# Kernel tuning notes

Hardware: AMD Instinct MI355X
Metric: run time of the kernel (lower is better)

The kernel has to match this reference:

```python
import jax, jax.numpy as jnp
import numpy as np

# ---- Cl(3,0) geometric-algebra Cayley table (8 blades: 1,e1,e2,e3,e12,e13,e23,e123) ----
# T[k, i, j] = sign s.t. blade_i * blade_j = sign * blade_k (exactly 8 (i,j) pairs per k).

def _build_cayley():
    masks = [0b000, 0b001, 0b010, 0b100, 0b011, 0b101, 0b110, 0b111]
    T = np.zeros((8, 8, 8), np.float32)
    for i, a in enumerate(masks):
        for j, b in enumerate(masks):
            k = masks.index(a ^ b)
            aa, s = a >> 1, 0
            while aa:
                s += bin(aa & b).count('1')
                aa >>= 1
            T[k, i, j] = -1.0 if (s & 1) else 1.0
    return jnp.asarray(T)

CAYLEY = _build_cayley()
LN_EPS = 1e-5  # torch LayerNorm default


def _layer_norm(x, w, b):
    mu = jnp.mean(x, axis=-1, keepdims=True)
    var = jnp.var(x, axis=-1, keepdims=True)
    return (x - mu) * jax.lax.rsqrt(var + LN_EPS) * w + b


def _expert_forward(x_e, p_in, p_out, iw, gg, w_gate, w_up, w_down, lnw, lnb, out_w, out_b):
    # x_e: (C, D); p_in: (D, ED); per-round params indexed [r]
    C = x_e.shape[0]
    DB = lnw.shape[-1]
    mv = (x_e @ p_in).reshape(C, 8, DB)  # (C, n_blades, d_blade)
    n_rounds = iw.shape[0]
    for r in range(n_rounds):
        w = jax.nn.sigmoid(iw[r]).reshape(8, 8)          # interaction weights w[i,j]
        gate = jax.nn.sigmoid(gg[r])                      # scalar geo gate
        # geo[n,k,d] = sum_{i,j} sign[k,i,j] * w[i,j] * mv[n,i,d] * mv[n,j,d]
        geo = jnp.einsum('kij,ij,nid,njd->nkd', CAYLEY, w, mv, mv)
        mixed = gate * geo + (1.0 - gate) * mv
        flat = _layer_norm(mixed, lnw[r], lnb[r])         # LN over d_blade
        h = jax.nn.silu(flat @ w_gate[r]) * (flat @ w_up[r])  # SwiGLU
        mv = mv + h @ w_down[r]                           # residual
    out = mv.reshape(C, -1) @ p_out                       # (C, D)
    return _layer_norm(out, out_w, out_b)


def setup_inputs() -> dict:
    key = jax.random.key(0)
    ks = jax.random.split(key, 8)
    E, D, NB, DB, R, F = 16, 1024, 8, 64, 2, 256
    ED = NB * DB
    N = 32768
    C = N // E
    std = 0.02
    return {
        'x_sorted': jax.random.normal(ks[0], (N, D), jnp.float32),
        'proj_in': jax.random.normal(ks[1], (E, D, ED), jnp.float32) * std,
        'proj_out': jax.random.normal(ks[2], (E, ED, D), jnp.float32) * std,
        'interaction_weights': jnp.ones((E, R, 64), jnp.float32) * 0.1,
        'geo_gates': jnp.ones((E, R), jnp.float32) * 0.5,
        'ffn_gate': jax.random.normal(ks[3], (E, R, DB, F), jnp.float32) * std,
        'ffn_up': jax.random.normal(ks[4], (E, R, DB, F), jnp.float32) * std,
        'ffn_down': jax.random.normal(ks[5], (E, R, F, DB), jnp.float32) * std,
        'ffn_ln_w': jnp.ones((E, R, DB), jnp.float32),
        'ffn_ln_b': jnp.zeros((E, R, DB), jnp.float32),
        'out_ln_w': jnp.ones((D,), jnp.float32),
        'out_ln_b': jnp.zeros((D,), jnp.float32),
        'expert_offsets': jnp.arange(E, dtype=jnp.int32) * C,
        'expert_counts': jnp.full((E,), C, dtype=jnp.int32),
    }


def reference(x_sorted, proj_in, proj_out, interaction_weights, geo_gates,
              ffn_gate, ffn_up, ffn_down, ffn_ln_w, ffn_ln_b,
              out_ln_w, out_ln_b, expert_offsets, expert_counts):
    E = proj_in.shape[0]
    N, D = x_sorted.shape
    C = N // E  # balanced routing: equal tokens per expert (static shapes)
    idx = expert_offsets[:, None].astype(jnp.int32) + jnp.arange(C, dtype=jnp.int32)[None, :]
    x_b = x_sorted[idx]  # (E, C, D) gather of sorted tokens per expert
    y_b = jax.vmap(_expert_forward,
                   in_axes=(0, 0, 0, 0, 0, 0, 0, 0, 0, 0, None, None))(
        x_b, proj_in, proj_out, interaction_weights, geo_gates,
        ffn_gate, ffn_up, ffn_down, ffn_ln_w, ffn_ln_b, out_ln_w, out_ln_b)
    y = jnp.zeros_like(x_sorted).at[idx.reshape(-1)].set(y_b.reshape(-1, D))
    return y
```

## Files before the change

kernel.cpp:

```cpp
#include <hip/hip_runtime.h>

#define DEV __device__ __forceinline__

typedef __attribute__((ext_vector_type(4))) float f32x4;
typedef __attribute__((ext_vector_type(2))) float f32x2;
typedef __attribute__((ext_vector_type(8))) short bf16x8;


DEV unsigned short f2bf(float f) {
  union { float f; unsigned u; } v; v.f = f;
  unsigned r = v.u + 0x7fffu + ((v.u >> 16) & 1u);
  return (unsigned short)(r >> 16);
}

DEV unsigned pk2bf(float lo, float hi) {
  unsigned r;
  asm("v_cvt_pk_bf16_f32 %0, %1, %2" : "=v"(r) : "v"(lo), "v"(hi));
  return r;
}
DEV unsigned short f2bf1(float v) { return (unsigned short)pk2bf(v, v); }

DEV float bf2f(unsigned short b) {
  union { unsigned u; float f; } v; v.u = ((unsigned)b) << 16; return v.f;
}

DEV float frcp(float x) { return __builtin_amdgcn_rcpf(x); }

DEV void sbar() { asm volatile("s_barrier" ::: "memory"); }
DEV void wait_lgkm0() { asm volatile("s_waitcnt lgkmcnt(0)" ::: "memory"); }
DEV void wait_vm0() { asm volatile("s_waitcnt vmcnt(0)" ::: "memory"); }

DEV void async16(const unsigned short* g, unsigned short* l) {
  __builtin_amdgcn_global_load_lds(
      (__attribute__((address_space(1))) const unsigned int*)g,
      (__attribute__((address_space(3))) unsigned int*)l, 16, 0, 0);
}

DEV long tiled_off(long n, int k, int K) {
  return (n >> 3) * (8L * K) + (long)(((k >> 3) * 64) + ((int)(n & 7)) * 8 + (k & 7));
}

DEV bf16x8 ld_frag(const char* s, int row, int hi) {
  return *(const bf16x8*)(s + ((row >> 3) * 512 + hi * 128 + (row & 7) * 16));
}

__host__ __device__ constexpr int km_(int i) { return i==0?0:i==1?1:i==2?2:i==3?4:i==4?3:i==5?5:i==6?6:7; }
__host__ __device__ constexpr int pc_(int x) { int c = 0; while (x) { c += x & 1; x >>= 1; } return c; }
__host__ __device__ constexpr int KIDX(int i, int j) { return km_(km_(i) ^ km_(j)); }
__host__ __device__ constexpr int CSGN(int i, int j) {
  int a = km_(i), b = km_(j), aa = a >> 1, s = 0;
  while (aa) { s += pc_(aa & b); aa >>= 1; }
  return (s & 1) ? -1 : 1;
}
__host__ __device__ constexpr int PIDX(int i, int j) {
  return 8 * i - (i * (i - 1)) / 2 + (j - i);
}


DEV void geoprep_body(const float* __restrict__ iw, const float* __restrict__ gg,
                      float* __restrict__ wcomb, int er) {
  const float* w = iw + er * 64;
  float gate = frcp(1.f + __expf(-gg[er]));
  float* c = wcomb + er * 40;
  int p = 0;
  for (int i = 0; i < 8; ++i)
    for (int j = i; j < 8; ++j) {
      float v = (float)CSGN(i, j) * frcp(1.f + __expf(-w[i * 8 + j]));
      if (j > i) v += (float)CSGN(j, i) * frcp(1.f + __expf(-w[j * 8 + i]));
      c[p++] = gate * v;
    }
  c[36] = 1.f - gate;
}

template<int TI>
DEV void transpose_body(const float* __restrict__ in, unsigned short* __restrict__ out,
                        int Rr, int Cc, int bx, int by, int bz, int tid, char* sbuf) {
  unsigned short (*tile)[33] = (unsigned short (*)[33])sbuf;
  const float* ib = in + (long)bz * Rr * Cc;
  unsigned short* ob = out + (long)bz * Rr * Cc;
  int r0 = by * 32, c0 = bx * 32;
  int tr = tid >> 5, tc = tid & 31;
#pragma unroll
  for (int i = 0; i < 4; ++i) {
    int r = tr + i * 8;
    tile[r][tc] = f2bf(ib[(long)(r0 + r) * Cc + c0 + tc]);
  }
  __syncthreads();
#pragma unroll
  for (int i = 0; i < 4; ++i) {
    int c = tr + i * 8;
    int row = c0 + c;
    int k = r0 + tc;
    if (TI == 0) ob[(long)row * Rr + k] = tile[tc][c];
    else ob[(long)row * Rr + (k ^ ((row & 7) << 3))] = tile[tc][c];
  }
}

DEV void trans_big_body(const float* __restrict__ in, unsigned short* __restrict__ out,
                        int Rr, int Cc, int bx, int by, int bz, int tid, char* sbuf) {
  float (*t)[64] = (float (*)[64])sbuf;
  const float* ib = in + (long)bz * Rr * Cc;
  unsigned short* ob = out + (long)bz * (long)Rr * Cc;
  int k0 = by * 64, n0 = bx * 64;
#pragma unroll
  for (int p = 0; p < 4; ++p) {
    int idx = p * 256 + tid;
    int kr = idx >> 4, nc = (idx & 15) * 4;
    *(float4*)&t[kr][nc] = *(const float4*)(ib + (long)(k0 + kr) * Cc + n0 + nc);
  }
  __syncthreads();
#pragma unroll
  for (int p = 0; p < 2; ++p) {
    int idx = p * 256 + tid;
    int n = idx & 63, kc = idx >> 6;
    float v[8];
#pragma unroll
    for (int u = 0; u < 8; ++u) v[u] = t[kc * 8 + u][n];
    uint4 o;
    o.x = pk2bf(v[0], v[1]); o.y = pk2bf(v[2], v[3]);
    o.z = pk2bf(v[4], v[5]); o.w = pk2bf(v[6], v[7]);
    *(uint4*)(ob + tiled_off(n0 + n, k0 + kc * 8, Rr)) = o;
  }
}

__global__ __launch_bounds__(256) void prep_k(
    const float* __restrict__ pin, const float* __restrict__ pout,
    const float* __restrict__ fg, const float* __restrict__ fu,
    const float* __restrict__ fd, const float* __restrict__ iw,
    const float* __restrict__ gg,
    unsigned short* __restrict__ pinT, unsigned short* __restrict__ poutT,
    unsigned short* __restrict__ wgT, unsigned short* __restrict__ wuT,
    unsigned short* __restrict__ wdT, float* __restrict__ wcomb) {
  __shared__ char sbuf[16384];
  int b = blockIdx.x, tid = threadIdx.x;
  if (b < 2048) {
    trans_big_body(pin, pinT, 1024, 512, b & 7, (b >> 3) & 15, b >> 7, tid, sbuf);
  } else if (b < 4096) {
    int j = b - 2048;
    trans_big_body(pout, poutT, 512, 1024, j & 15, (j >> 4) & 7, j >> 7, tid, sbuf);
  } else if (b < 4608) {
    int j = b - 4096;
    transpose_body<1>(fg, wgT, 64, 256, j & 7, (j >> 3) & 1, j >> 4, tid, sbuf);
  } else if (b < 5120) {
    int j = b - 4608;
    transpose_body<1>(fu, wuT, 64, 256, j & 7, (j >> 3) & 1, j >> 4, tid, sbuf);
  } else if (b < 5632) {
    int j = b - 5120;
    transpose_body<0>(fd, wdT, 256, 64, j & 1, (j >> 1) & 7, j >> 4, tid, sbuf);
  } else {
    if (tid < 32) geoprep_body(iw, gg, wcomb, tid);
  }
}

__global__ __launch_bounds__(512, 1) void gemm_in_k(const float* __restrict__ X,
                                                    const unsigned short* __restrict__ Bw,
                                                    unsigned short* __restrict__ MvB,
                                                    const int* __restrict__ offs) {
  extern __shared__ char smem[];
  int bid = blockIdx.x;
  int wg = (bid & 7) * 32 + (bid >> 3);
  int e = wg >> 4, rem = wg & 15, bm = rem >> 1, bn = rem & 1;
  int tid = threadIdx.x, wid = tid >> 6, lane = tid & 63;
  int wm = (wid >> 2) * 128, wn = (wid & 3) * 64;
  int ri = lane & 15, hi = lane >> 4;
  long rowbase = (long)offs[e] + bm * 256;
  long bw = (long)e * 64 + bn * 32;

  auto STGB = [&](int p) {
    int t = p >> 1, s = p & 1, b = t & 1;
    char* dst = smem + b * 65536 + 32768 + s * 16384;
#pragma unroll
    for (int i = 0; i < 2; ++i) {
      int d = i * 512 + tid;
      async16(Bw + (bw + (d >> 5)) * 8192 +
                  (long)((t * 8 + s * 4 + ((d >> 3) & 3)) * 64 + (d & 7) * 8),
              (unsigned short*)(dst + d * 16));
    }
  };
  auto A_LOAD = [&](int p, float4 ar[2][2]) {
    int t = p >> 1, s = p & 1;
#pragma unroll
    for (int i = 0; i < 2; ++i) {
      int d = i * 512 + tid;
      const float* src = X + (rowbase + ((d >> 5) * 8 + (d & 7))) * 1024 +
                         t * 64 + s * 32 + ((d >> 3) & 3) * 8;
      ar[i][0] = *(const float4*)src;
      ar[i][1] = *(const float4*)(src + 4);
    }
  };
  auto A_WRITE = [&](int p, float4 ar[2][2]) {
    int t = p >> 1, s = p & 1, b = t & 1;
    char* dst = smem + b * 65536 + s * 16384;
#pragma unroll
    for (int i = 0; i < 2; ++i) {
      int d = i * 512 + tid;
      uint4 o;
      o.x = pk2bf(ar[i][0].x, ar[i][0].y);
      o.y = pk2bf(ar[i][0].z, ar[i][0].w);
      o.z = pk2bf(ar[i][1].x, ar[i][1].y);
      o.w = pk2bf(ar[i][1].z, ar[i][1].w);
      *(uint4*)(dst + d * 16) = o;
    }
  };

  f32x4 acc[8][4];
#pragma unroll
  for (int i = 0; i < 8; ++i)
#pragma unroll
    for (int j = 0; j < 4; ++j) acc[i][j] = (f32x4){0.f, 0.f, 0.f, 0.f};

  float4 ar[2][2];
  A_LOAD(0, ar); STGB(0); STGB(1);
  A_WRITE(0, ar);
  A_LOAD(1, ar);
  A_WRITE(1, ar);
  wait_lgkm0();

#pragma unroll 2
  for (int p = 0; p < 32; ++p) {
    int t = p >> 1, s = p & 1, c = t & 1;
    if (p < 30) { A_LOAD(p + 2, ar); STGB(p + 2); }
    if (p < 30) asm volatile("s_waitcnt vmcnt(8)" ::: "memory");
    else if (p == 30) asm volatile("s_waitcnt vmcnt(2)" ::: "memory");
    else asm volatile("s_waitcnt vmcnt(0)" ::: "memory");
    sbar();
    const char* cA = smem + c * 65536 + s * 16384;
    const char* cB = smem + c * 65536 + 32768 + s * 16384;
    bf16x8 a[8], b[4];
#pragma unroll
    for (int i = 0; i < 8; ++i) a[i] = ld_frag(cA, wm + i * 16 + ri, hi);
#pragma unroll
    for (int j = 0; j < 4; ++j) b[j] = ld_frag(cB, wn + j * 16 + ri, hi);
    __builtin_amdgcn_s_setprio(1);
#pragma unroll
    for (int i = 0; i < 8; ++i)
#pragma unroll
      for (int j = 0; j < 4; ++j)
        acc[i][j] = __builtin_amdgcn_mfma_f32_16x16x32_bf16(a[i], b[j], acc[i][j], 0, 0, 0);
    __builtin_amdgcn_s_setprio(0);
    if (p < 30) A_WRITE(p + 2, ar);
    wait_lgkm0();
  }

  unsigned short* Cb = MvB + ((long)e * 2048 + (long)bm * 256) * 512 + bn * 256;
#pragma unroll
  for (int i = 0; i < 8; ++i)
#pragma unroll
    for (int j = 0; j < 4; ++j)
#pragma unroll
      for (int rr = 0; rr < 4; ++rr)
        Cb[(long)(wm + i * 16 + hi * 4 + rr) * 512 + wn + j * 16 + ri] =
            f2bf1(acc[i][j][rr]);
}

__global__ __launch_bounds__(256, 2) void rounds_k(
    const unsigned short* __restrict__ MvB, const unsigned short* __restrict__ WgT,
    const unsigned short* __restrict__ WuT, const unsigned short* __restrict__ WdT,
    const float* __restrict__ wcomb, const float* __restrict__ lnw,
    const float* __restrict__ lnb, unsigned short* __restrict__ Mvb) {
  extern __shared__ char smem[];
  int tid = threadIdx.x, wid = tid >> 6, lane = tid & 63;
  char* sFH = smem + wid * 8192;
  char* sMv = smem + 32768 + wid * 8192;
  char* sW  = smem + 65536;

  int bid = blockIdx.x;
  int wg = (bid & 7) * 128 + (bid >> 3);
  int e = wg >> 6, bx = wg & 63;

  int t8 = lane >> 3, q = lane & 7;
  int ri = lane & 15, hi = lane >> 4;
  int sw = (ri & 7) << 4;

  auto STAGE = [&](int i8) {
    long base = (long)(e * 2 + (i8 >> 3)) * 16384 + (i8 & 7) * 2048;
    char* dst = sW + (i8 & 1) * 8192;
    async16(WgT + base + tid * 8, (unsigned short*)(dst + tid * 16));
    async16(WuT + base + tid * 8, (unsigned short*)(dst + 4096 + tid * 16));
  };
  STAGE(0);

#pragma unroll 1
  for (int r = 0; r < 2; ++r) {
    int er = e * 2 + r;
    const unsigned short* wd = WdT + (long)er * 16384;

    f32x4 mv[2][8];
    if (r == 0) {
      long base = ((long)e * 2048 + bx * 32 + wid * 8 + t8) * 512 + 8 * q;
      uint4 uv[8];
#pragma unroll
      for (int i = 0; i < 8; ++i)
        uv[i] = *(const uint4*)(MvB + base + i * 64);
#pragma unroll
      for (int i = 0; i < 8; ++i) {
        *(uint4*)(sMv + t8 * 1024 + i * 128 + ((16 * q) ^ (i << 4))) = uv[i];
        mv[0][i] = (f32x4){bf2f((unsigned short)(uv[i].x & 0xffff)),
                           bf2f((unsigned short)(uv[i].x >> 16)),
                           bf2f((unsigned short)(uv[i].y & 0xffff)),
                           bf2f((unsigned short)(uv[i].y >> 16))};
        mv[1][i] = (f32x4){bf2f((unsigned short)(uv[i].z & 0xffff)),
                           bf2f((unsigned short)(uv[i].z >> 16)),
                           bf2f((unsigned short)(uv[i].w & 0xffff)),
                           bf2f((unsigned short)(uv[i].w >> 16))};
      }
    } else {
#pragma unroll
      for (int i = 0; i < 8; ++i) {
        uint4 uv = *(const uint4*)(sMv + t8 * 1024 + i * 128 + ((16 * q) ^ (i << 4)));
        mv[0][i] = (f32x4){bf2f((unsigned short)(uv.x & 0xffff)),
                           bf2f((unsigned short)(uv.x >> 16)),
                           bf2f((unsigned short)(uv.y & 0xffff)),
                           bf2f((unsigned short)(uv.y >> 16))};
        mv[1][i] = (f32x4){bf2f((unsigned short)(uv.z & 0xffff)),
                           bf2f((unsigned short)(uv.z >> 16)),
                           bf2f((unsigned short)(uv.w & 0xffff)),
                           bf2f((unsigned short)(uv.w >> 16))};
      }
    }

    {
      const float* C = wcomb + er * 40;
      f32x4 g[2][8];
#pragma unroll
      for (int hf = 0; hf < 2; ++hf)
#pragma unroll
        for (int k = 0; k < 8; ++k) g[hf][k] = (f32x4){0.f, 0.f, 0.f, 0.f};
#pragma unroll
      for (int i = 0; i < 8; ++i)
#pragma unroll
        for (int j = i; j < 8; ++j) {
          float cc = C[PIDX(i, j)];
          const int k = KIDX(i, j);
          g[0][k] += cc * (mv[0][i] * mv[0][j]);
          g[1][k] += cc * (mv[1][i] * mv[1][j]);
        }
      float omg = C[36];
#pragma unroll
      for (int hf = 0; hf < 2; ++hf)
#pragma unroll
        for (int k = 0; k < 8; ++k) g[hf][k] = omg * mv[hf][k] + g[hf][k];
      float4 lwa = *(const float4*)(lnw + (long)er * 64 + 8 * q);
      float4 lwb = *(const float4*)(lnw + (long)er * 64 + 8 * q + 4);
      float4 lba = *(const float4*)(lnb + (long)er * 64 + 8 * q);
      float4 lbb = *(const float4*)(lnb + (long)er * 64 + 8 * q + 4);
      f32x4 lwvA = (f32x4){lwa.x, lwa.y, lwa.z, lwa.w};
      f32x4 lwvB = (f32x4){lwb.x, lwb.y, lwb.z, lwb.w};
      f32x4 lbvA = (f32x4){lba.x, lba.y, lba.z, lba.w};
      f32x4 lbvB = (f32x4){lbb.x, lbb.y, lbb.z, lbb.w};
#pragma unroll
      for (int bh = 0; bh < 2; ++bh) {
        f32x2 red[4];
#pragma unroll
        for (int k = 0; k < 4; ++k) {
          f32x4 a = g[0][bh * 4 + k], b = g[1][bh * 4 + k];
          red[k].x = ((a.x + a.y) + (a.z + a.w)) + ((b.x + b.y) + (b.z + b.w));
          red[k].y = (fmaf(a.x, a.x, a.y * a.y) + fmaf(a.z, a.z, a.w * a.w)) +
                     (fmaf(b.x, b.x, b.y * b.y) + fmaf(b.z, b.z, b.w * b.w));
        }
#pragma unroll
        for (int off = 4; off >= 1; off >>= 1)
#pragma unroll
          for (int t = 0; t < 4; ++t) {
            f32x2 o;
            o.x = __shfl_xor(red[t].x, off);
            o.y = __shfl_xor(red[t].y, off);
            red[t] += o;
          }
#pragma unroll
        for (int k = 0; k < 4; ++k) {
          int kk = bh * 4 + k;
          float mean = red[k].x * (1.f / 64.f);
          float var = red[k].y * (1.f / 64.f) - mean * mean;
          float rs = rsqrtf(var + 1e-5f);
          f32x4 ovA = ((g[0][kk] - mean) * rs) * lwvA + lbvA;
          f32x4 ovB = ((g[1][kk] - mean) * rs) * lwvB + lbvB;
          uint4 pv;
          pv.x = pk2bf(ovA.x, ovA.y);
          pv.y = pk2bf(ovA.z, ovA.w);
          pv.z = pk2bf(ovB.x, ovB.y);
          pv.w = pk2bf(ovB.z, ovB.w);
          int row = t8 * 8 + kk;
          *(uint4*)(sFH + row * 128 + ((16 * q) ^ (kk << 4))) = pv;
        }
      }
    }
    wait_lgkm0();

    bf16x8 bfr[4][2];
#pragma unroll
    for (int tt = 0; tt < 4; ++tt)
#pragma unroll
      for (int kt = 0; kt < 2; ++kt)
        bfr[tt][kt] = *(const bf16x8*)(sFH + (tt * 16 + ri) * 128 + ((kt * 64 + hi * 16) ^ sw));

    f32x4 acc2[4][4];
#pragma unroll
    for (int j = 0; j < 4; ++j)
#pragma unroll
      for (int tt = 0; tt < 4; ++tt) acc2[j][tt] = (f32x4){0.f, 0.f, 0.f, 0.f};

#pragma unroll 1
    for (int q8 = 0; q8 < 8; ++q8) {
      int i8 = r * 8 + q8;
      wait_vm0();
      sbar();
      if (i8 < 15) STAGE(i8 + 1);

      bf16x8 wdf[4];
#pragma unroll
      for (int j = 0; j < 4; ++j)
        wdf[j] = *(const bf16x8*)(wd + (j * 16 + ri) * 256 + q8 * 32 + hi * 8);

      const char* bufW = sW + (i8 & 1) * 8192;

#pragma unroll
      for (int ftl = 0; ftl < 2; ++ftl) {
        const char* bg = bufW + (ftl * 16 + ri) * 128;
        const char* bu = bg + 4096;
        bf16x8 wg0 = *(const bf16x8*)(bg + ((hi * 16) ^ sw));
        bf16x8 wg1 = *(const bf16x8*)(bg + ((64 + hi * 16) ^ sw));
        bf16x8 wu0 = *(const bf16x8*)(bu + ((hi * 16) ^ sw));
        bf16x8 wu1 = *(const bf16x8*)(bu + ((64 + hi * 16) ^ sw));
        f32x4 ag[4], au[4];
#pragma unroll
        for (int tt = 0; tt < 4; ++tt) {
          ag[tt] = (f32x4){0.f, 0.f, 0.f, 0.f};
          au[tt] = (f32x4){0.f, 0.f, 0.f, 0.f};
        }
        __builtin_amdgcn_s_setprio(1);
#pragma unroll
        for (int tt = 0; tt < 4; ++tt) {
          ag[tt] = __builtin_amdgcn_mfma_f32_16x16x32_bf16(wg0, bfr[tt][0], ag[tt], 0, 0, 0);
          au[tt] = __builtin_amdgcn_mfma_f32_16x16x32_bf16(wu0, bfr[tt][0], au[tt], 0, 0, 0);
          ag[tt] = __builtin_amdgcn_mfma_f32_16x16x32_bf16(wg1, bfr[tt][1], ag[tt], 0, 0, 0);
          au[tt] = __builtin_amdgcn_mfma_f32_16x16x32_bf16(wu1, bfr[tt][1], au[tt], 0, 0, 0);
        }
        __builtin_amdgcn_s_setprio(0);
#pragma unroll
        for (int tt = 0; tt < 4; ++tt) {
          float hh[4];
#pragma unroll
          for (int rr = 0; rr < 4; ++rr) {
            float gv = ag[tt][rr], uu = au[tt][rr];
            hh[rr] = gv * uu * frcp(1.f + __expf(-gv));
          }
          uint2 hwv;
          hwv.x = pk2bf(hh[0], hh[1]);
          hwv.y = pk2bf(hh[2], hh[3]);
          *(uint2*)(sFH + (tt * 16 + ri) * 128 + ((ftl * 32 + hi * 8) ^ sw)) = hwv;
        }
      }
      wait_lgkm0();

      bf16x8 hk[4];
#pragma unroll
      for (int tt = 0; tt < 4; ++tt)
        hk[tt] = *(const bf16x8*)(sFH + (tt * 16 + ri) * 128 + ((hi * 16) ^ sw));
      __builtin_amdgcn_s_setprio(1);
#pragma unroll
      for (int j = 0; j < 4; ++j)
#pragma unroll
        for (int tt = 0; tt < 4; ++tt)
          acc2[j][tt] = __builtin_amdgcn_mfma_f32_16x16x32_bf16(wdf[j], hk[tt], acc2[j][tt], 0, 0, 0);
      __builtin_amdgcn_s_setprio(0);
    }

    {
#pragma unroll
      for (int tt = 0; tt < 4; ++tt) {
        int tl = tt * 2 + (ri >> 3);
        int kb = ri & 7;
#pragma unroll
        for (int j = 0; j < 4; ++j)
#pragma unroll
          for (int u = 0; u < 2; ++u) {
            int off = (j * 32 + hi * 8 + 4 * u) ^ sw;
            unsigned* p = (unsigned*)(sMv + tl * 1024 + kb * 128 + off);
            unsigned old = *p;
            float v0 = bf2f((unsigned short)(old & 0xffff)) + acc2[j][tt][2 * u];
            float v1 = bf2f((unsigned short)(old >> 16)) + acc2[j][tt][2 * u + 1];
            *p = pk2bf(v0, v1);
          }
      }
    }
    wait_lgkm0();

    if (r == 1) {
      int bl = lane >> 3, qq = lane & 7;
      long sbase = ((long)e * 2048 + bx * 32 + wid * 8) * 512;
#pragma unroll
      for (int h = 0; h < 8; ++h) {
        uint4 v = *(const uint4*)(sMv + h * 1024 + bl * 128 + ((16 * qq) ^ (bl << 4)));
        *(uint4*)(Mvb + sbase + h * 512 + lane * 8) = v;
      }
    }
  }
}

__global__ __launch_bounds__(512, 2) void gemm_out_ln_k(
    const unsigned short* __restrict__ Mvb, const unsigned short* __restrict__ Pw,
    float* __restrict__ Out, const float* __restrict__ ow, const float* __restrict__ ob,
    const int* __restrict__ offs) {
  extern __shared__ char smem[];
  int bid = blockIdx.x;
  int wg = (bid & 7) * 64 + (bid >> 3);
  int e = wg >> 5, mb = wg & 31;
  int tid = threadIdx.x, wid = tid >> 6, lane = tid & 63;
  int ri = lane & 15, hi = lane >> 4;
  long bbase = (long)e * 524288;
  long arow0 = (long)e * 2048 + (long)mb * 64;

  auto STAGE = [&](int buf, int kt) {
#pragma unroll
    for (int i = 0; i < 8; ++i) {
      int q = i * 512 + tid;
      int w = q >> 5, c = (q >> 3) & 3, rr = q & 7;
      async16(Pw + bbase + (long)w * 4096 + (kt * 4 + c) * 64 + rr * 8,
              (unsigned short*)(smem + buf * 65536 + q * 16));
    }
    if (tid < 256) {
      int q = tid;
      int w = q >> 5, c = (q >> 3) & 3, rr = q & 7;
      async16(Mvb + (arow0 + w * 8 + rr) * 512 + kt * 32 + c * 8,
              (unsigned short*)(smem + 131072 + buf * 4096 + q * 16));
    }
  };

  f32x4 acc[4][8];
#pragma unroll
  for (int i = 0; i < 4; ++i)
#pragma unroll
    for (int j = 0; j < 8; ++j) acc[i][j] = (f32x4){0.f, 0.f, 0.f, 0.f};

  STAGE(0, 0);
  for (int kt = 0; kt < 16; ++kt) {
    int cur = kt & 1;
    if (kt < 15) {
      STAGE(cur ^ 1, kt + 1);
      asm volatile("s_waitcnt vmcnt(8)" ::: "memory");
    } else {
      asm volatile("s_waitcnt vmcnt(0)" ::: "memory");
    }
    sbar();
    const char* cB = smem + cur * 65536;
    const char* cA = smem + 131072 + cur * 4096;
    bf16x8 a[4], b[8];
#pragma unroll
    for (int i = 0; i < 4; ++i) a[i] = ld_frag(cA, i * 16 + ri, hi);
#pragma unroll
    for (int j = 0; j < 8; ++j) b[j] = ld_frag(cB, wid * 128 + j * 16 + ri, hi);
    __builtin_amdgcn_s_setprio(1);
#pragma unroll
    for (int i = 0; i < 4; ++i)
#pragma unroll
      for (int j = 0; j < 8; ++j)
        acc[i][j] = __builtin_amdgcn_mfma_f32_16x16x32_bf16(a[i], b[j], acc[i][j], 0, 0, 0);
    __builtin_amdgcn_s_setprio(0);
    sbar();
  }

  float* rsum = (float*)(smem + 139264);
  float* rsq  = (float*)(smem + 141312);
  float* mexp = (float*)(smem + 143360);
  float* rstd = (float*)(smem + 143616);
  int hi4 = hi * 4;
#pragma unroll
  for (int i = 0; i < 4; ++i)
#pragma unroll
    for (int rr = 0; rr < 4; ++rr) {
      float s = 0.f, qv = 0.f;
#pragma unroll
      for (int j = 0; j < 8; ++j) { float v = acc[i][j][rr]; s += v; qv += v * v; }
#pragma unroll
      for (int off = 1; off < 16; off <<= 1) {
        s += __shfl_xor(s, off);
        qv += __shfl_xor(qv, off);
      }
      if (ri == 0) {
        int row = i * 16 + hi4 + rr;
        rsum[row * 8 + wid] = s;
        rsq[row * 8 + wid] = qv;
      }
    }
  __syncthreads();
  if (tid < 64) {
    float S = 0.f, Q = 0.f;
#pragma unroll
    for (int w = 0; w < 8; ++w) { S += rsum[tid * 8 + w]; Q += rsq[tid * 8 + w]; }
    float mean = S * (1.f / 1024.f);
    float var = Q * (1.f / 1024.f) - mean * mean;
    mexp[tid] = mean;
    rstd[tid] = rsqrtf(var + 1e-5f);
  }
  __syncthreads();
  long r0 = (long)offs[e] + (long)mb * 64;
  float owv[8], obv[8];
#pragma unroll
  for (int j = 0; j < 8; ++j) {
    int col = wid * 128 + j * 16 + ri;
    owv[j] = ow[col];
    obv[j] = ob[col];
  }
#pragma unroll
  for (int i = 0; i < 4; ++i)
#pragma unroll
    for (int rr = 0; rr < 4; ++rr) {
      int row = i * 16 + hi4 + rr;
      float mu = mexp[row], rs = rstd[row];
#pragma unroll
      for (int j = 0; j < 8; ++j) {
        int col = wid * 128 + j * 16 + ri;
        Out[(r0 + row) * 1024 + col] = (acc[i][j][rr] - mu) * rs * owv[j] + obv[j];
      }
    }
}

extern "C" void kernel_launch(void* const* d_in, const int* in_sizes, int n_in,
                              void* d_out, int out_size, void* d_ws, size_t ws_size,
                              hipStream_t stream) {
  const float* x    = (const float*)d_in[0];
  const float* pin  = (const float*)d_in[1];
  const float* pout = (const float*)d_in[2];
  const float* iw   = (const float*)d_in[3];
  const float* gg   = (const float*)d_in[4];
  const float* fg   = (const float*)d_in[5];
  const float* fu   = (const float*)d_in[6];
  const float* fd   = (const float*)d_in[7];
  const float* lnw  = (const float*)d_in[8];
  const float* lnb  = (const float*)d_in[9];
  const float* ow   = (const float*)d_in[10];
  const float* ob   = (const float*)d_in[11];
  const int* offs   = (const int*)d_in[12];

  char* ws = (char*)d_ws;
  unsigned short* mvB  = (unsigned short*)(ws + 0L);
  unsigned short* mvb  = (unsigned short*)(ws + 33554432L);
  unsigned short* pinT = (unsigned short*)(ws + 67108864L);
  unsigned short* poutT= (unsigned short*)(ws + 83886080L);
  unsigned short* wgT  = (unsigned short*)(ws + 100663296L);
  unsigned short* wuT  = (unsigned short*)(ws + 102760448L);
  unsigned short* wdT  = (unsigned short*)(ws + 104857600L);
  float* wcomb         = (float*)(ws + 106954752L);

  prep_k<<<dim3(5633), dim3(256), 0, stream>>>(
      pin, pout, fg, fu, fd, iw, gg, pinT, poutT, wgT, wuT, wdT, wcomb);

  gemm_in_k<<<dim3(256), dim3(512), 131072, stream>>>(x, pinT, mvB, offs);

  rounds_k<<<dim3(1024), dim3(256), 81920, stream>>>(
      mvB, wgT, wuT, wdT, wcomb, lnw, lnb, mvb);

  gemm_out_ln_k<<<dim3(512), dim3(512), 143872, stream>>>(
      mvb, poutT, (float*)d_out, ow, ob, offs);
}
```

Before: 253.1 us.

## Keep multivector state in registers, drop sMv LDS buffer, raise rounds_k occupancy

The rounds kernel now keeps each thread's bf16 multivector slice in registers (uv) across both rounds instead of a dedicated 32KB LDS buffer. The down-projection delta is staged through the existing sFH scratch region, then read back in the owning thread's layout and added to the register copy. The final write goes straight from registers to global memory. Dropping the buffer cuts LDS from 80KB to 48KB and raises launch bounds to 3 blocks per CU, aiming for more occupancy. In exchange the delta takes an extra bf16 rounding step, and register pressure rises under the tighter register budget, which risks spills.

Measured after the change: 313.7 us. 24.0% more time.

```diff
diff --git a/kernel.cpp b/kernel.cpp
--- a/kernel.cpp
+++ b/kernel.cpp
@@ -253,7 +253,7 @@
             f2bf1(acc[i][j][rr]);
 }
 
-__global__ __launch_bounds__(256, 2) void rounds_k(
+__global__ __launch_bounds__(256, 3) void rounds_k(
     const unsigned short* __restrict__ MvB, const unsigned short* __restrict__ WgT,
     const unsigned short* __restrict__ WuT, const unsigned short* __restrict__ WdT,
     const float* __restrict__ wcomb, const float* __restrict__ lnw,
@@ -261,8 +261,7 @@
   extern __shared__ char smem[];
   int tid = threadIdx.x, wid = tid >> 6, lane = tid & 63;
   char* sFH = smem + wid * 8192;
-  char* sMv = smem + 32768 + wid * 8192;
-  char* sW  = smem + 65536;
+  char* sW  = smem + 32768;
 
   int bid = blockIdx.x;
   int wg = (bid & 7) * 128 + (bid >> 3);
@@ -280,43 +279,30 @@
   };
   STAGE(0);
 
+  uint4 uv[8];
+  {
+    long base = ((long)e * 2048 + bx * 32 + wid * 8 + t8) * 512 + 8 * q;
+#pragma unroll
+    for (int i = 0; i < 8; ++i)
+      uv[i] = *(const uint4*)(MvB + base + i * 64);
+  }
+
 #pragma unroll 1
   for (int r = 0; r < 2; ++r) {
     int er = e * 2 + r;
     const unsigned short* wd = WdT + (long)er * 16384;
 
     f32x4 mv[2][8];
-    if (r == 0) {
-      long base = ((long)e * 2048 + bx * 32 + wid * 8 + t8) * 512 + 8 * q;
-      uint4 uv[8];
-#pragma unroll
-      for (int i = 0; i < 8; ++i)
-        uv[i] = *(const uint4*)(MvB + base + i * 64);
-#pragma unroll
-      for (int i = 0; i < 8; ++i) {
-        *(uint4*)(sMv + t8 * 1024 + i * 128 + ((16 * q) ^ (i << 4))) = uv[i];
-        mv[0][i] = (f32x4){bf2f((unsigned short)(uv[i].x & 0xffff)),
-                           bf2f((unsigned short)(uv[i].x >> 16)),
-                           bf2f((unsigned short)(uv[i].y & 0xffff)),
-                           bf2f((unsigned short)(uv[i].y >> 16))};
-        mv[1][i] = (f32x4){bf2f((unsigned short)(uv[i].z & 0xffff)),
-                           bf2f((unsigned short)(uv[i].z >> 16)),
-                           bf2f((unsigned short)(uv[i].w & 0xffff)),
-                           bf2f((unsigned short)(uv[i].w >> 16))};
-      }
-    } else {
-#pragma unroll
-      for (int i = 0; i < 8; ++i) {
-        uint4 uv = *(const uint4*)(sMv + t8 * 1024 + i * 128 + ((16 * q) ^ (i << 4)));
-        mv[0][i] = (f32x4){bf2f((unsigned short)(uv.x & 0xffff)),
-                           bf2f((unsigned short)(uv.x >> 16)),
-                           bf2f((unsigned short)(uv.y & 0xffff)),
-                           bf2f((unsigned short)(uv.y >> 16))};
-        mv[1][i] = (f32x4){bf2f((unsigned short)(uv.z & 0xffff)),
-                           bf2f((unsigned short)(uv.z >> 16)),
-                           bf2f((unsigned short)(uv.w & 0xffff)),
-                           bf2f((unsigned short)(uv.w >> 16))};
-      }
+#pragma unroll
+    for (int i = 0; i < 8; ++i) {
+      mv[0][i] = (f32x4){bf2f((unsigned short)(uv[i].x & 0xffff)),
+                         bf2f((unsigned short)(uv[i].x >> 16)),
+                         bf2f((unsigned short)(uv[i].y & 0xffff)),
+                         bf2f((unsigned short)(uv[i].y >> 16))};
+      mv[1][i] = (f32x4){bf2f((unsigned short)(uv[i].z & 0xffff)),
+                         bf2f((unsigned short)(uv[i].z >> 16)),
+                         bf2f((unsigned short)(uv[i].w & 0xffff)),
+                         bf2f((unsigned short)(uv[i].w >> 16))};
     }
 
     {
@@ -472,28 +458,37 @@
         int tl = tt * 2 + (ri >> 3);
         int kb = ri & 7;
 #pragma unroll
-        for (int j = 0; j < 4; ++j)
-#pragma unroll
-          for (int u = 0; u < 2; ++u) {
-            int off = (j * 32 + hi * 8 + 4 * u) ^ sw;
-            unsigned* p = (unsigned*)(sMv + tl * 1024 + kb * 128 + off);
-            unsigned old = *p;
-            float v0 = bf2f((unsigned short)(old & 0xffff)) + acc2[j][tt][2 * u];
-            float v1 = bf2f((unsigned short)(old >> 16)) + acc2[j][tt][2 * u + 1];
-            *p = pk2bf(v0, v1);
-          }
+        for (int j = 0; j < 4; ++j) {
+          uint2 dv;
+          dv.x = pk2bf(acc2[j][tt][0], acc2[j][tt][1]);
+          dv.y = pk2bf(acc2[j][tt][2], acc2[j][tt][3]);
+          *(uint2*)(sFH + tl * 1024 + kb * 128 + ((j * 32 + hi * 8) ^ sw)) = dv;
+        }
       }
+      wait_lgkm0();
+#pragma unroll
+      for (int i = 0; i < 8; ++i) {
+        uint4 dv = *(const uint4*)(sFH + t8 * 1024 + i * 128 + ((16 * q) ^ (i << 4)));
+        unsigned* up = (unsigned*)&uv[i];
+        const unsigned* dp = (const unsigned*)&dv;
+#pragma unroll
+        for (int w = 0; w < 4; ++w) {
+          float a0 = bf2f((unsigned short)(up[w] & 0xffff)) +
+                     bf2f((unsigned short)(dp[w] & 0xffff));
+          float a1 = bf2f((unsigned short)(up[w] >> 16)) +
+                     bf2f((unsigned short)(dp[w] >> 16));
+          up[w] = pk2bf(a0, a1);
+        }
+      }
     }
     wait_lgkm0();
 
     if (r == 1) {
-      int bl = lane >> 3, qq = lane & 7;
-      long sbase = ((long)e * 2048 + bx * 32 + wid * 8) * 512;
-#pragma unroll
-      for (int h = 0; h < 8; ++h) {
-        uint4 v = *(const uint4*)(sMv + h * 1024 + bl * 128 + ((16 * qq) ^ (bl << 4)));
-        *(uint4*)(Mvb + sbase + h * 512 + lane * 8) = v;
-      }
+      long row = (long)e * 2048 + bx * 32 + wid * 8 + t8;
+      unsigned short* dst = Mvb + row * 512 + 8 * q;
+#pragma unroll
+      for (int i = 0; i < 8; ++i)
+        *(uint4*)(dst + i * 64) = uv[i];
     }
   }
 }
@@ -648,7 +643,7 @@
 
   gemm_in_k<<<dim3(256), dim3(512), 131072, stream>>>(x, pinT, mvB, offs);
 
-  rounds_k<<<dim3(1024), dim3(256), 81920, stream>>>(
+  rounds_k<<<dim3(1024), dim3(256), 49152, stream>>>(
       mvB, wgT, wuT, wdT, wcomb, lnw, lnb, mvb);
 
   gemm_out_ln_k<<<dim3(512), dim3(512), 143872, stream>>>(
```
